# Kernel tuning notes

Hardware: AMD Instinct MI355X
Metric: run time of the kernel (lower is better)

The kernel has to match this reference:

```python
import jax, jax.numpy as jnp
import numpy as np

N_NODES = 50000
N_EDGES = 600000
N_GRAPHS = 64
IN_C, HID_C, OUT_C = 128, 128, 64


def gcn_conv(x, edge_index, W, b, num_nodes):
    """PyG GCNConv: x' = D^-1/2 (A + I) D^-1/2 (x W) + b, messages src->dst."""
    src, dst = edge_index[0], edge_index[1]
    # add self-loops
    loop = jnp.arange(num_nodes, dtype=src.dtype)
    src_full = jnp.concatenate([src, loop])
    dst_full = jnp.concatenate([dst, loop])
    # degree of A+I counted at the aggregation (dst) side
    deg = jax.ops.segment_sum(jnp.ones_like(dst_full, dtype=x.dtype), dst_full,
                              num_segments=num_nodes)
    dinv = jax.lax.rsqrt(jnp.maximum(deg, 1.0))
    norm = dinv[src_full] * dinv[dst_full]              # [E+N]
    h = x @ W                                           # [N, C_out] dense GEMM
    msg = h[src_full] * norm[:, None]                   # gather + scale
    out = jax.ops.segment_sum(msg, dst_full, num_segments=num_nodes)  # scatter-add
    return out + b


def global_mean_pool(x, batch, num_graphs):
    s = jax.ops.segment_sum(x, batch, num_segments=num_graphs)
    cnt = jax.ops.segment_sum(jnp.ones_like(batch, dtype=x.dtype), batch,
                              num_segments=num_graphs)
    return s / jnp.maximum(cnt, 1.0)[:, None]


def setup_inputs() -> dict:
    key = jax.random.key(0)
    ks = jax.random.split(key, 8)
    x = jax.random.normal(ks[0], (N_NODES, IN_C), dtype=jnp.float32)
    edge_index = jax.random.randint(ks[1], (2, N_EDGES), 0, N_NODES, dtype=jnp.int64)
    batch = jnp.sort(jax.random.randint(ks[2], (N_NODES,), 0, N_GRAPHS, dtype=jnp.int64))
    # Glorot-style init like PyG defaults
    W1 = jax.random.normal(ks[3], (IN_C, HID_C), dtype=jnp.float32) * (1.0 / np.sqrt(IN_C))
    b1 = jnp.zeros((HID_C,), dtype=jnp.float32)
    W2 = jax.random.normal(ks[4], (HID_C, OUT_C), dtype=jnp.float32) * (1.0 / np.sqrt(HID_C))
    b2 = jnp.zeros((OUT_C,), dtype=jnp.float32)
    return {"x": x, "W1": W1, "b1": b1, "W2": W2, "b2": b2,
            "edge_index": edge_index, "batch": batch}


def reference(x, W1, b1, W2, b2, edge_index, batch):
    h = gcn_conv(x, edge_index, W1, b1, N_NODES)
    h = jax.nn.relu(h)
    h = gcn_conv(h, edge_index, W2, b2, N_NODES)
    return global_mean_pool(h, batch, N_GRAPHS)  # [N_GRAPHS, OUT_C]
```

## Files before the change

kernel.cpp:

```cpp
#include <hip/hip_runtime.h>

#define NN 50000
#define NE 600000
#define NG 64
#define SCAN_T 1024
#define SCAN_NB ((NN + SCAN_T - 1) / SCAN_T)

typedef unsigned int uint_t;
typedef unsigned short ushort_t;
typedef __attribute__((ext_vector_type(8))) short bf16x8;
typedef __attribute__((ext_vector_type(4))) float f32x4;

__device__ __forceinline__ ushort_t f2bf(float x) {
    uint_t u = __builtin_bit_cast(uint_t, x);
    u = (u + 0x7FFFu + ((u >> 16) & 1u)) >> 16;
    return (ushort_t)u;
}
__device__ __forceinline__ float bf_lo(uint_t p) {
    uint_t v = p << 16; return __builtin_bit_cast(float, v);
}
__device__ __forceinline__ float bf_hi(uint_t p) {
    uint_t v = p & 0xFFFF0000u; return __builtin_bit_cast(float, v);
}

__global__ void k_prep(const float* __restrict__ W1, const float* __restrict__ W2,
                       int* __restrict__ deg, float* __restrict__ psum,
                       ushort_t* __restrict__ W1t, ushort_t* __restrict__ W2t) {
    int i = blockIdx.x * blockDim.x + threadIdx.x;
    if (i < NN) deg[i] = 0;
    if (i < NG * 64) psum[i] = 0.f;
    if (i < 128 * 128) {
        int k = i >> 7, n = i & 127;
        W1t[n * 128 + k] = f2bf(W1[i]);
    }
    if (i < 128 * 64) {
        int k = i >> 6, n = i & 63;
        W2t[n * 128 + k] = f2bf(W2[i]);
    }
}

__global__ void k_hist(const int* __restrict__ dst, int* __restrict__ deg) {
    int e = blockIdx.x * blockDim.x + threadIdx.x;
    if (e < NE) atomicAdd(&deg[dst[e]], 1);
}

__global__ __launch_bounds__(SCAN_T) void k_scan1(const int* __restrict__ deg,
                                                  int* __restrict__ blockSums) {
    __shared__ int s[SCAN_T];
    int i = blockIdx.x * SCAN_T + threadIdx.x;
    s[threadIdx.x] = (i < NN) ? deg[i] : 0;
    __syncthreads();
    for (int off = SCAN_T / 2; off > 0; off >>= 1) {
        if (threadIdx.x < off) s[threadIdx.x] += s[threadIdx.x + off];
        __syncthreads();
    }
    if (threadIdx.x == 0) blockSums[blockIdx.x] = s[0];
}

__global__ __launch_bounds__(SCAN_T) void k_scan3(const int* __restrict__ deg,
                                                  const int* __restrict__ blockSums,
                                                  int* __restrict__ rowptr,
                                                  int* __restrict__ cursor,
                                                  float* __restrict__ dinv) {
    __shared__ int offs[64];
    __shared__ int s[SCAN_T];
    const int t = threadIdx.x;
    if (t < 64) {
        int orig = (t < SCAN_NB) ? blockSums[t] : 0;
        int v = orig;
        for (int off = 1; off < 64; off <<= 1) {
            int u = __shfl_up(v, off);
            if (t >= off) v += u;
        }
        offs[t] = v - orig;
    }
    const int i = blockIdx.x * SCAN_T + t;
    const int v = (i < NN) ? deg[i] : 0;
    s[t] = v;
    __syncthreads();
    for (int off = 1; off < SCAN_T; off <<= 1) {
        int u = (t >= off) ? s[t - off] : 0;
        int cur = s[t];
        __syncthreads();
        s[t] = cur + u;
        __syncthreads();
    }
    if (i < NN) {
        int ex = offs[blockIdx.x] + s[t] - v;
        rowptr[i] = ex;
        cursor[i] = ex;
        dinv[i] = rsqrtf((float)(v + 1));
    }
    if (i == 0) rowptr[NN] = NE;
}

__global__ void k_scatter(const int* __restrict__ src, const int* __restrict__ dst,
                          int* __restrict__ cursor, int* __restrict__ csr_src) {
    int e = blockIdx.x * blockDim.x + threadIdx.x;
    if (e >= NE) return;
    int d = dst[e];
    int p = atomicAdd(&cursor[d], 1);
    csr_src[p] = src[e];
}

__global__ __launch_bounds__(256) void k_gemm_mfma(const float* __restrict__ X,
                                                   const ushort_t* __restrict__ Wt,
                                                   const float* __restrict__ dinv,
                                                   ushort_t* __restrict__ Hb) {
    __shared__ ushort_t xs[128 * 128];
    __shared__ ushort_t ws[128 * 128];
    const int tid = threadIdx.x;
    const int row0 = blockIdx.x * 128;

    for (int idx = tid; idx < 128 * 32; idx += 256) {
        int r = idx >> 5, c4 = idx & 31;
        int row = row0 + r;
        float4 v = make_float4(0.f, 0.f, 0.f, 0.f);
        if (row < NN) v = ((const float4*)X)[(long)row * 32 + c4];
        ushort4 o;
        o.x = f2bf(v.x); o.y = f2bf(v.y); o.z = f2bf(v.z); o.w = f2bf(v.w);
        uint_t byte = (uint_t)(r * 256 + c4 * 8) ^ (uint_t)((r & 7) << 4);
        *(ushort4*)((char*)xs + byte) = o;
    }
    for (int idx = tid; idx < 128 * 16; idx += 256) {
        int n = idx >> 4, c16 = idx & 15;
        uint4 v = ((const uint4*)Wt)[idx];
        uint_t byte = (uint_t)(n * 256 + c16 * 16) ^ (uint_t)((n & 7) << 4);
        *(uint4*)((char*)ws + byte) = v;
    }
    __syncthreads();

    const int w = tid >> 6;
    const int l = tid & 63;
    const int m0 = (w >> 1) * 4;
    const int n0 = (w & 1) * 4;
    const int lr = l & 15;
    const int kg = l >> 4;

    f32x4 acc[4][4] = {};
    for (int kk = 0; kk < 4; ++kk) {
        const int kb = kk * 64 + kg * 16;
        bf16x8 a[4], b[4];
#pragma unroll
        for (int m = 0; m < 4; ++m) {
            int r = (m0 + m) * 16 + lr;
            uint_t byte = (uint_t)(r * 256 + kb) ^ (uint_t)((r & 7) << 4);
            a[m] = *(const bf16x8*)((const char*)xs + byte);
        }
#pragma unroll
        for (int n = 0; n < 4; ++n) {
            int r = (n0 + n) * 16 + lr;
            uint_t byte = (uint_t)(r * 256 + kb) ^ (uint_t)((r & 7) << 4);
            b[n] = *(const bf16x8*)((const char*)ws + byte);
        }
#pragma unroll
        for (int m = 0; m < 4; ++m)
#pragma unroll
            for (int n = 0; n < 4; ++n)
                acc[m][n] = __builtin_amdgcn_mfma_f32_16x16x32_bf16(a[m], b[n], acc[m][n], 0, 0, 0);
    }

#pragma unroll
    for (int m = 0; m < 4; ++m) {
#pragma unroll
        for (int r = 0; r < 4; ++r) {
            int row = row0 + (m0 + m) * 16 + kg * 4 + r;
            if (row < NN) {
                float sc = dinv[row];
#pragma unroll
                for (int n = 0; n < 4; ++n) {
                    int col = (n0 + n) * 16 + lr;
                    Hb[(long)row * 128 + col] = f2bf(acc[m][n][r] * sc);
                }
            }
        }
    }
}

__global__ __launch_bounds__(256) void k_agg1g2(const int* __restrict__ rowptr,
                                                const int* __restrict__ csr_src,
                                                const float* __restrict__ dinv,
                                                const ushort_t* __restrict__ Hb,
                                                const float* __restrict__ bias,
                                                const ushort_t* __restrict__ W2t,
                                                ushort_t* __restrict__ G) {
    constexpr int TPN = 8;
    constexpr int NPB = 32;
    __shared__ ushort_t hsh[NPB * 128];
    __shared__ ushort_t ws2[64 * 128];
    const int tid = threadIdx.x;
    const int row0 = blockIdx.x * NPB;
    const int nodeLocal = tid / TPN;
    const int node = row0 + nodeLocal;
    const int lane = tid % TPN;

    for (int idx = tid; idx < 64 * 16; idx += 256) {
        int n = idx >> 4, c16 = idx & 15;
        uint4 v = ((const uint4*)W2t)[idx];
        uint_t byte = (uint_t)(n * 256 + c16 * 16) ^ (uint_t)((n & 7) << 4);
        *(uint4*)((char*)ws2 + byte) = v;
    }

    float a[16];
    if (node < NN) {
        const float dd = dinv[node];
        const uint2* __restrict__ H2 = (const uint2*)Hb;
        const long base = (long)node * 32;
#pragma unroll
        for (int q = 0; q < 4; ++q) {
            uint2 h = H2[base + lane * 4 + q];
            a[q * 4 + 0] = bf_lo(h.x); a[q * 4 + 1] = bf_hi(h.x);
            a[q * 4 + 2] = bf_lo(h.y); a[q * 4 + 3] = bf_hi(h.y);
        }
        const int beg = rowptr[node], end = rowptr[node + 1];
        int k = beg;
        const int n2 = beg + ((end - beg) & ~1);
        for (; k < n2; k += 2) {
            long b0 = (long)csr_src[k] * 16 + lane * 2;
            long b1 = (long)csr_src[k + 1] * 16 + lane * 2;
            uint4 h0 = ((const uint4*)Hb)[b0];
            uint4 h1 = ((const uint4*)Hb)[b0 + 1];
            uint4 h2 = ((const uint4*)Hb)[b1];
            uint4 h3 = ((const uint4*)Hb)[b1 + 1];
            a[0] += bf_lo(h0.x) + bf_lo(h2.x); a[1] += bf_hi(h0.x) + bf_hi(h2.x);
            a[2] += bf_lo(h0.y) + bf_lo(h2.y); a[3] += bf_hi(h0.y) + bf_hi(h2.y);
            a[4] += bf_lo(h0.z) + bf_lo(h2.z); a[5] += bf_hi(h0.z) + bf_hi(h2.z);
            a[6] += bf_lo(h0.w) + bf_lo(h2.w); a[7] += bf_hi(h0.w) + bf_hi(h2.w);
            a[8]  += bf_lo(h1.x) + bf_lo(h3.x); a[9]  += bf_hi(h1.x) + bf_hi(h3.x);
            a[10] += bf_lo(h1.y) + bf_lo(h3.y); a[11] += bf_hi(h1.y) + bf_hi(h3.y);
            a[12] += bf_lo(h1.z) + bf_lo(h3.z); a[13] += bf_hi(h1.z) + bf_hi(h3.z);
            a[14] += bf_lo(h1.w) + bf_lo(h3.w); a[15] += bf_hi(h1.w) + bf_hi(h3.w);
        }
        for (; k < end; ++k) {
            long b0 = (long)csr_src[k] * 16 + lane * 2;
            uint4 h0 = ((const uint4*)Hb)[b0];
            uint4 h1 = ((const uint4*)Hb)[b0 + 1];
            a[0] += bf_lo(h0.x); a[1] += bf_hi(h0.x);
            a[2] += bf_lo(h0.y); a[3] += bf_hi(h0.y);
            a[4] += bf_lo(h0.z); a[5] += bf_hi(h0.z);
            a[6] += bf_lo(h0.w); a[7] += bf_hi(h0.w);
            a[8]  += bf_lo(h1.x); a[9]  += bf_hi(h1.x);
            a[10] += bf_lo(h1.y); a[11] += bf_hi(h1.y);
            a[12] += bf_lo(h1.z); a[13] += bf_hi(h1.z);
            a[14] += bf_lo(h1.w); a[15] += bf_hi(h1.w);
        }
#pragma unroll
        for (int q = 0; q < 4; ++q) {
            float4 bb = *(const float4*)&bias[lane * 16 + q * 4];
            float v0 = fmaxf(a[q * 4 + 0] * dd + bb.x, 0.f);
            float v1 = fmaxf(a[q * 4 + 1] * dd + bb.y, 0.f);
            float v2 = fmaxf(a[q * 4 + 2] * dd + bb.z, 0.f);
            float v3 = fmaxf(a[q * 4 + 3] * dd + bb.w, 0.f);
            ushort4 o;
            o.x = f2bf(v0); o.y = f2bf(v1); o.z = f2bf(v2); o.w = f2bf(v3);
            uint_t byte = (uint_t)(nodeLocal * 256 + lane * 32 + q * 8)
                        ^ (uint_t)((nodeLocal & 7) << 4);
            *(ushort4*)((char*)hsh + byte) = o;
        }
    } else {
#pragma unroll
        for (int q = 0; q < 4; ++q) {
            ushort4 o = {0, 0, 0, 0};
            uint_t byte = (uint_t)(nodeLocal * 256 + lane * 32 + q * 8)
                        ^ (uint_t)((nodeLocal & 7) << 4);
            *(ushort4*)((char*)hsh + byte) = o;
        }
    }
    __syncthreads();

    const int w = tid >> 6;
    const int l = tid & 63;
    const int lr = l & 15;
    const int kg = l >> 4;
    const int mt = w >> 1;
    const int nt0 = (w & 1) * 2;

    f32x4 acc[2] = {};
    for (int kk = 0; kk < 4; ++kk) {
        const int kb = kk * 64 + kg * 16;
        int ra = mt * 16 + lr;
        uint_t ba = (uint_t)(ra * 256 + kb) ^ (uint_t)((ra & 7) << 4);
        bf16x8 afrag = *(const bf16x8*)((const char*)hsh + ba);
#pragma unroll
        for (int j = 0; j < 2; ++j) {
            int rb = (nt0 + j) * 16 + lr;
            uint_t bb = (uint_t)(rb * 256 + kb) ^ (uint_t)((rb & 7) << 4);
            bf16x8 bfrag = *(const bf16x8*)((const char*)ws2 + bb);
            acc[j] = __builtin_amdgcn_mfma_f32_16x16x32_bf16(afrag, bfrag, acc[j], 0, 0, 0);
        }
    }

    float sc[4];
    int rowb = row0 + mt * 16 + kg * 4;
#pragma unroll
    for (int r = 0; r < 4; ++r) sc[r] = (rowb + r < NN) ? dinv[rowb + r] : 0.f;
#pragma unroll
    for (int j = 0; j < 2; ++j) {
        int col = (nt0 + j) * 16 + lr;
#pragma unroll
        for (int r = 0; r < 4; ++r) {
            int row = rowb + r;
            if (row < NN) G[(long)row * 64 + col] = f2bf(acc[j][r] * sc[r]);
        }
    }
}

__global__ __launch_bounds__(256) void k_agg2pool(const int* __restrict__ rowptr,
                                                  const int* __restrict__ csr_src,
                                                  const float* __restrict__ dinv,
                                                  const ushort_t* __restrict__ Gb,
                                                  const int* __restrict__ batch,
                                                  float* __restrict__ psum) {
    constexpr int TPN = 8;
    constexpr int NPB = 32;
    const int nodeLocal = threadIdx.x / TPN;
    const int node = blockIdx.x * NPB + nodeLocal;
    const int lane = threadIdx.x % TPN;
    __shared__ float vsh[NPB][64 + 1];
    __shared__ int gsh[NPB];

    if (node < NN) {
        const float dd = dinv[node];
        const uint4* __restrict__ H4 = (const uint4*)Gb;

        float a0, a1, a2, a3, a4, a5, a6, a7;
        {
            uint4 sv = H4[(long)node * TPN + lane];
            a0 = bf_lo(sv.x); a1 = bf_hi(sv.x);
            a2 = bf_lo(sv.y); a3 = bf_hi(sv.y);
            a4 = bf_lo(sv.z); a5 = bf_hi(sv.z);
            a6 = bf_lo(sv.w); a7 = bf_hi(sv.w);
        }
        const int beg = rowptr[node], end = rowptr[node + 1];
        int k = beg;
        const int n4 = beg + ((end - beg) & ~3);
        for (; k < n4; k += 4) {
            int s0 = csr_src[k + 0];
            int s1 = csr_src[k + 1];
            int s2 = csr_src[k + 2];
            int s3 = csr_src[k + 3];
            uint4 h0 = H4[(long)s0 * TPN + lane];
            uint4 h1 = H4[(long)s1 * TPN + lane];
            uint4 h2 = H4[(long)s2 * TPN + lane];
            uint4 h3 = H4[(long)s3 * TPN + lane];
            a0 += (bf_lo(h0.x) + bf_lo(h1.x)) + (bf_lo(h2.x) + bf_lo(h3.x));
            a1 += (bf_hi(h0.x) + bf_hi(h1.x)) + (bf_hi(h2.x) + bf_hi(h3.x));
            a2 += (bf_lo(h0.y) + bf_lo(h1.y)) + (bf_lo(h2.y) + bf_lo(h3.y));
            a3 += (bf_hi(h0.y) + bf_hi(h1.y)) + (bf_hi(h2.y) + bf_hi(h3.y));
            a4 += (bf_lo(h0.z) + bf_lo(h1.z)) + (bf_lo(h2.z) + bf_lo(h3.z));
            a5 += (bf_hi(h0.z) + bf_hi(h1.z)) + (bf_hi(h2.z) + bf_hi(h3.z));
            a6 += (bf_lo(h0.w) + bf_lo(h1.w)) + (bf_lo(h2.w) + bf_lo(h3.w));
            a7 += (bf_hi(h0.w) + bf_hi(h1.w)) + (bf_hi(h2.w) + bf_hi(h3.w));
        }
        for (; k < end; ++k) {
            int s = csr_src[k];
            uint4 h = H4[(long)s * TPN + lane];
            a0 += bf_lo(h.x); a1 += bf_hi(h.x);
            a2 += bf_lo(h.y); a3 += bf_hi(h.y);
            a4 += bf_lo(h.z); a5 += bf_hi(h.z);
            a6 += bf_lo(h.w); a7 += bf_hi(h.w);
        }
        float* vp = &vsh[nodeLocal][lane * 8];
        vp[0] = a0 * dd; vp[1] = a1 * dd; vp[2] = a2 * dd; vp[3] = a3 * dd;
        vp[4] = a4 * dd; vp[5] = a5 * dd; vp[6] = a6 * dd; vp[7] = a7 * dd;
        if (lane == 0) gsh[nodeLocal] = batch[node];
    } else {
        if (lane == 0) gsh[nodeLocal] = -1;
    }
    __syncthreads();

    if (threadIdx.x < 64) {
        const int ch = threadIdx.x;
        float acc = 0.f;
        int gprev = -1;
        for (int n = 0; n < NPB; ++n) {
            int g = gsh[n];
            if (g != gprev) {
                if (gprev >= 0) unsafeAtomicAdd(&psum[gprev * 64 + ch], acc);
                acc = 0.f;
                gprev = g;
            }
            if (g >= 0) acc += vsh[n][ch];
        }
        if (gprev >= 0) unsafeAtomicAdd(&psum[gprev * 64 + ch], acc);
    }
}

__global__ __launch_bounds__(64) void k_pool2(const float* __restrict__ psum,
                                              const int* __restrict__ batch,
                                              const float* __restrict__ b2,
                                              float* __restrict__ out) {
    const int g = blockIdx.x;
    const int ch = threadIdx.x;
    int beg, end;
    {
        int lo = 0, hi = NN;
        while (lo < hi) { int mid = (lo + hi) >> 1; if (batch[mid] < g) lo = mid + 1; else hi = mid; }
        beg = lo;
        lo = beg; hi = NN;
        while (lo < hi) { int mid = (lo + hi) >> 1; if (batch[mid] < g + 1) lo = mid + 1; else hi = mid; }
        end = lo;
    }
    int cnt = end - beg;
    out[g * 64 + ch] = (cnt > 0) ? (psum[g * 64 + ch] / (float)cnt + b2[ch]) : 0.f;
}

extern "C" void kernel_launch(void* const* d_in, const int* in_sizes, int n_in,
                              void* d_out, int out_size, void* d_ws, size_t ws_size,
                              hipStream_t stream) {
    const float* x  = (const float*)d_in[0];
    const float* W1 = (const float*)d_in[1];
    const float* b1 = (const float*)d_in[2];
    const float* W2 = (const float*)d_in[3];
    const float* b2 = (const float*)d_in[4];
    const int* ei   = (const int*)d_in[5];
    const int* src  = (const int*)ei;
    const int* dst  = (const int*)(ei + NE);
    const int* batch = (const int*)d_in[6];
    float* out = (float*)d_out;

    char* p = (char*)d_ws;
    int* deg       = (int*)p;          p += (size_t)NN * 4;
    int* rowptr    = (int*)p;          p += (size_t)(NN + 4) * 4;
    int* cursor    = (int*)p;          p += (size_t)NN * 4;
    int* csr_src   = (int*)p;          p += (size_t)NE * 4;
    int* blockSums = (int*)p;          p += (size_t)64 * 4;
    float* dinv    = (float*)p;        p += (size_t)NN * 4;
    float* psum    = (float*)p;        p += (size_t)NG * 64 * 4;
    ushort_t* W1t  = (ushort_t*)p;     p += (size_t)128 * 128 * 2;
    ushort_t* W2t  = (ushort_t*)p;     p += (size_t)64 * 128 * 2;
    ushort_t* Hb   = (ushort_t*)p;     p += (size_t)NN * 128 * 2;
    ushort_t* Gb   = (ushort_t*)p;     p += (size_t)NN * 64 * 2;

    k_prep<<<(NN + 255) / 256, 256, 0, stream>>>(W1, W2, deg, psum, W1t, W2t);
    k_hist<<<(NE + 255) / 256, 256, 0, stream>>>(dst, deg);
    k_scan1<<<SCAN_NB, SCAN_T, 0, stream>>>(deg, blockSums);
    k_scan3<<<SCAN_NB, SCAN_T, 0, stream>>>(deg, blockSums, rowptr, cursor, dinv);
    k_scatter<<<(NE + 255) / 256, 256, 0, stream>>>(src, dst, cursor, csr_src);

    k_gemm_mfma<<<(NN + 127) / 128, 256, 0, stream>>>(x, W1t, dinv, Hb);

    k_agg1g2<<<(NN + 31) / 32, 256, 0, stream>>>(rowptr, csr_src, dinv, Hb, b1, W2t, Gb);

    k_agg2pool<<<(NN + 31) / 32, 256, 0, stream>>>(rowptr, csr_src, dinv, Gb, batch, psum);

    k_pool2<<<NG, 64, 0, stream>>>(psum, batch, b2, out);
}
```

Baseline: 153.7 us.

## Merge two-pass scan into single-pass decoupled scan and enlarge agg1g2 blocks

Replaces the two scan kernels with one kernel in which each block publishes its sum through flag words and waits on the flags of earlier blocks. Spare blocks in the same launch take over the weight transpose and bf16 conversion and the psum zeroing that k_prep used to do, which saves a launch. The spin-wait assumes every scan block is resident at the same time, which holds for 49 blocks but is a forward-progress risk. Separately, k_agg1g2 now runs 64 nodes per 512-thread block, spreading the W2 shared-memory load over more nodes at the cost of more LDS per block.

```diff
diff --git a/kernel.cpp b/kernel.cpp
--- a/kernel.cpp
+++ b/kernel.cpp
@@ -5,6 +5,7 @@
 #define NG 64
 #define SCAN_T 1024
 #define SCAN_NB ((NN + SCAN_T - 1) / SCAN_T)
+#define SCANX_NB 64
 
 typedef unsigned int uint_t;
 typedef unsigned short ushort_t;
@@ -23,20 +24,10 @@
     uint_t v = p & 0xFFFF0000u; return __builtin_bit_cast(float, v);
 }
 
-__global__ void k_prep(const float* __restrict__ W1, const float* __restrict__ W2,
-                       int* __restrict__ deg, float* __restrict__ psum,
-                       ushort_t* __restrict__ W1t, ushort_t* __restrict__ W2t) {
+__global__ void k_prep(int* __restrict__ deg, int* __restrict__ scanflags) {
     int i = blockIdx.x * blockDim.x + threadIdx.x;
     if (i < NN) deg[i] = 0;
-    if (i < NG * 64) psum[i] = 0.f;
-    if (i < 128 * 128) {
-        int k = i >> 7, n = i & 127;
-        W1t[n * 128 + k] = f2bf(W1[i]);
-    }
-    if (i < 128 * 64) {
-        int k = i >> 6, n = i & 63;
-        W2t[n * 128 + k] = f2bf(W2[i]);
-    }
+    if (i < SCANX_NB) scanflags[i] = 0;
 }
 
 __global__ void k_hist(const int* __restrict__ dst, int* __restrict__ deg) {
@@ -44,49 +35,67 @@
     if (e < NE) atomicAdd(&deg[dst[e]], 1);
 }
 
-__global__ __launch_bounds__(SCAN_T) void k_scan1(const int* __restrict__ deg,
-                                                  int* __restrict__ blockSums) {
-    __shared__ int s[SCAN_T];
-    int i = blockIdx.x * SCAN_T + threadIdx.x;
-    s[threadIdx.x] = (i < NN) ? deg[i] : 0;
-    __syncthreads();
-    for (int off = SCAN_T / 2; off > 0; off >>= 1) {
-        if (threadIdx.x < off) s[threadIdx.x] += s[threadIdx.x + off];
-        __syncthreads();
-    }
-    if (threadIdx.x == 0) blockSums[blockIdx.x] = s[0];
-}
-
-__global__ __launch_bounds__(SCAN_T) void k_scan3(const int* __restrict__ deg,
-                                                  const int* __restrict__ blockSums,
+__global__ __launch_bounds__(SCAN_T) void k_scanx(const int* __restrict__ deg,
+                                                  const float* __restrict__ W1,
+                                                  const float* __restrict__ W2,
+                                                  int* __restrict__ scanflags,
                                                   int* __restrict__ rowptr,
                                                   int* __restrict__ cursor,
-                                                  float* __restrict__ dinv) {
-    __shared__ int offs[64];
+                                                  float* __restrict__ dinv,
+                                                  ushort_t* __restrict__ W1t,
+                                                  ushort_t* __restrict__ W2t,
+                                                  float* __restrict__ psum) {
+    const int b = blockIdx.x;
+    const int tid = threadIdx.x;
+
+    if (b >= SCAN_NB) {
+        int idx = (b - SCAN_NB) * SCAN_T + tid;
+        for (int i = idx; i < 128 * 128; i += (SCANX_NB - SCAN_NB) * SCAN_T) {
+            int k = i >> 7, n = i & 127;
+            W1t[n * 128 + k] = f2bf(W1[i]);
+        }
+        if (idx < 128 * 64) {
+            int k = idx >> 6, n = idx & 63;
+            W2t[n * 128 + k] = f2bf(W2[idx]);
+        }
+        if (idx < NG * 64) psum[idx] = 0.f;
+        return;
+    }
+
     __shared__ int s[SCAN_T];
-    const int t = threadIdx.x;
-    if (t < 64) {
-        int orig = (t < SCAN_NB) ? blockSums[t] : 0;
-        int v = orig;
-        for (int off = 1; off < 64; off <<= 1) {
-            int u = __shfl_up(v, off);
-            if (t >= off) v += u;
-        }
-        offs[t] = v - orig;
-    }
-    const int i = blockIdx.x * SCAN_T + t;
+    __shared__ int offs_s;
+    const int i = b * SCAN_T + tid;
     const int v = (i < NN) ? deg[i] : 0;
-    s[t] = v;
+    s[tid] = v;
     __syncthreads();
     for (int off = 1; off < SCAN_T; off <<= 1) {
-        int u = (t >= off) ? s[t - off] : 0;
-        int cur = s[t];
+        int u = (tid >= off) ? s[tid - off] : 0;
+        int cur = s[tid];
         __syncthreads();
-        s[t] = cur + u;
+        s[tid] = cur + u;
         __syncthreads();
     }
+    if (tid == SCAN_T - 1) {
+        __hip_atomic_store(&scanflags[b], s[SCAN_T - 1] | (int)0x80000000,
+                           __ATOMIC_RELEASE, __HIP_MEMORY_SCOPE_AGENT);
+    }
+    if (tid < 64) {
+        int w = 0;
+        if (tid < b) {
+            int f;
+            do {
+                f = __hip_atomic_load(&scanflags[tid], __ATOMIC_ACQUIRE,
+                                      __HIP_MEMORY_SCOPE_AGENT);
+            } while (!(f & (int)0x80000000));
+            w = f & 0x7FFFFFFF;
+        }
+        for (int off = 32; off > 0; off >>= 1) w += __shfl_down(w, off);
+        if (tid == 0) offs_s = w;
+    }
+    __syncthreads();
+
     if (i < NN) {
-        int ex = offs[blockIdx.x] + s[t] - v;
+        int ex = offs_s + s[tid] - v;
         rowptr[i] = ex;
         cursor[i] = ex;
         dinv[i] = rsqrtf((float)(v + 1));
@@ -177,7 +186,7 @@
     }
 }
 
-__global__ __launch_bounds__(256) void k_agg1g2(const int* __restrict__ rowptr,
+__global__ __launch_bounds__(512) void k_agg1g2(const int* __restrict__ rowptr,
                                                 const int* __restrict__ csr_src,
                                                 const float* __restrict__ dinv,
                                                 const ushort_t* __restrict__ Hb,
@@ -185,7 +194,7 @@
                                                 const ushort_t* __restrict__ W2t,
                                                 ushort_t* __restrict__ G) {
     constexpr int TPN = 8;
-    constexpr int NPB = 32;
+    constexpr int NPB = 64;
     __shared__ ushort_t hsh[NPB * 128];
     __shared__ ushort_t ws2[64 * 128];
     const int tid = threadIdx.x;
@@ -194,7 +203,7 @@
     const int node = row0 + nodeLocal;
     const int lane = tid % TPN;
 
-    for (int idx = tid; idx < 64 * 16; idx += 256) {
+    for (int idx = tid; idx < 64 * 16; idx += 512) {
         int n = idx >> 4, c16 = idx & 15;
         uint4 v = ((const uint4*)W2t)[idx];
         uint_t byte = (uint_t)(n * 256 + c16 * 16) ^ (uint_t)((n & 7) << 4);
@@ -424,7 +433,7 @@
     int* rowptr    = (int*)p;          p += (size_t)(NN + 4) * 4;
     int* cursor    = (int*)p;          p += (size_t)NN * 4;
     int* csr_src   = (int*)p;          p += (size_t)NE * 4;
-    int* blockSums = (int*)p;          p += (size_t)64 * 4;
+    int* scanflags = (int*)p;          p += (size_t)SCANX_NB * 4;
     float* dinv    = (float*)p;        p += (size_t)NN * 4;
     float* psum    = (float*)p;        p += (size_t)NG * 64 * 4;
     ushort_t* W1t  = (ushort_t*)p;     p += (size_t)128 * 128 * 2;
@@ -432,15 +441,15 @@
     ushort_t* Hb   = (ushort_t*)p;     p += (size_t)NN * 128 * 2;
     ushort_t* Gb   = (ushort_t*)p;     p += (size_t)NN * 64 * 2;
 
-    k_prep<<<(NN + 255) / 256, 256, 0, stream>>>(W1, W2, deg, psum, W1t, W2t);
+    k_prep<<<(NN + 255) / 256, 256, 0, stream>>>(deg, scanflags);
     k_hist<<<(NE + 255) / 256, 256, 0, stream>>>(dst, deg);
-    k_scan1<<<SCAN_NB, SCAN_T, 0, stream>>>(deg, blockSums);
-    k_scan3<<<SCAN_NB, SCAN_T, 0, stream>>>(deg, blockSums, rowptr, cursor, dinv);
+    k_scanx<<<SCANX_NB, SCAN_T, 0, stream>>>(deg, W1, W2, scanflags, rowptr, cursor,
+                                             dinv, W1t, W2t, psum);
     k_scatter<<<(NE + 255) / 256, 256, 0, stream>>>(src, dst, cursor, csr_src);
 
     k_gemm_mfma<<<(NN + 127) / 128, 256, 0, stream>>>(x, W1t, dinv, Hb);
 
-    k_agg1g2<<<(NN + 31) / 32, 256, 0, stream>>>(rowptr, csr_src, dinv, Hb, b1, W2t, Gb);
+    k_agg1g2<<<(NN + 63) / 64, 512, 0, stream>>>(rowptr, csr_src, dinv, Hb, b1, W2t, Gb);
 
     k_agg2pool<<<(NN + 31) / 32, 256, 0, stream>>>(rowptr, csr_src, dinv, Gb, batch, psum);
 
```

After: 154.1 us. No clear change (+0.3%).
